# Kernel optimization log

Hardware: AMD Instinct MI355X
Metric: run time of the kernel (lower is better)

Reference implementation:

```python
import jax, jax.numpy as jnp
import numpy as np

V, H, L, B, S = 32000, 1024, 2, 8, 256


def setup_inputs() -> dict:
    key = jax.random.key(0)
    ks = jax.random.split(key, 12)
    s = 1.0 / np.sqrt(H)  # PyTorch LSTM/Linear init range
    u = lambda k, shape: jax.random.uniform(k, shape, jnp.float32, -s, s)
    return {
        "x": jax.random.randint(ks[0], (B, S), 0, V, dtype=jnp.int32),
        "h0": jnp.zeros((L, B, H), jnp.float32),
        "c0": jnp.zeros((L, B, H), jnp.float32),
        "w_ih0": u(ks[1], (4 * H, V)),
        "w_hh0": u(ks[2], (4 * H, H)),
        "b_ih0": u(ks[3], (4 * H,)),
        "b_hh0": u(ks[4], (4 * H,)),
        "w_ih1": u(ks[5], (4 * H, H)),
        "w_hh1": u(ks[6], (4 * H, H)),
        "b_ih1": u(ks[7], (4 * H,)),
        "b_hh1": u(ks[8], (4 * H,)),
        "fc_w": u(ks[9], (V, H)),
        "fc_b": u(ks[10], (V,)),
    }


def _lstm_layer(xproj, h0, c0, w_hh):
    """xproj: [S,B,4H] input-to-gate projection (biases folded in).
    Gate order i,f,g,o matches PyTorch."""
    def step(carry, xp):
        h, c = carry
        g = xp + h @ w_hh.T  # [B,4H]
        i, f, gg, o = jnp.split(g, 4, axis=-1)
        c = jax.nn.sigmoid(f) * c + jax.nn.sigmoid(i) * jnp.tanh(gg)
        h = jax.nn.sigmoid(o) * jnp.tanh(c)
        return (h, c), h
    (hT, cT), hs = jax.lax.scan(step, (h0, c0), xproj)
    return hs, hT, cT


def reference(x, h0, c0, w_ih0, w_hh0, b_ih0, b_hh0, w_ih1, w_hh1, b_ih1, b_hh1, fc_w, fc_b):
    # F.one_hot(x, V).float() @ w_ih0.T  ==  gather of rows of w_ih0.T (identical math)
    xp0 = jnp.take(w_ih0.T, x, axis=0) + (b_ih0 + b_hh0)  # [B,S,4H]
    xp0 = xp0.transpose(1, 0, 2)  # [S,B,4H] for time-major scan
    h1s, h1T, c1T = _lstm_layer(xp0, h0[0], c0[0], w_hh0)
    xp1 = h1s @ w_ih1.T + (b_ih1 + b_hh1)  # [S,B,4H]
    h2s, h2T, c2T = _lstm_layer(xp1, h0[1], c0[1], w_hh1)
    out = h2s.transpose(1, 0, 2).reshape(-1, H)  # [B*S,H]
    logits = out @ fc_w.T + fc_b  # [B*S,V]
    hn = jnp.stack([h1T, h2T])
    cn = jnp.stack([c1T, c2T])
    return logits, (hn, cn)
```

## Files before the change

kernel.cpp:

```cpp
#include <hip/hip_runtime.h>
#include <cmath>

typedef float  f32x4  __attribute__((ext_vector_type(4)));
typedef float  f32x2  __attribute__((ext_vector_type(2)));
typedef __bf16 bf16x8 __attribute__((ext_vector_type(8)));

static constexpr int HN  = 1024;
static constexpr int VN  = 32000;
static constexpr int BN  = 8;
static constexpr int SN  = 256;
static constexpr int H4N = 4096;

__global__ __launch_bounds__(256) void k_gather(const int* __restrict__ x,
    const float* __restrict__ w_ih0, const float* __restrict__ b_ih0,
    const float* __restrict__ b_hh0, float* __restrict__ xpB) {
  int t = blockIdx.x;
  __shared__ int toks[8];
  if (threadIdx.x < 8) toks[threadIdx.x] = x[threadIdx.x * SN + t];
  __syncthreads();
  int wgx = threadIdx.x;
  for (int g = 0; g < 4; ++g) {
    float vals[4][8];
    #pragma unroll
    for (int u = 0; u < 4; ++u) {
      int row = g * 1024 + wgx * 4 + u;
      float bias = b_ih0[row] + b_hh0[row];
      const float* wr = w_ih0 + (size_t)row * VN;
      #pragma unroll
      for (int b = 0; b < 8; ++b) vals[u][b] = wr[toks[b]] + bias;
    }
    float* dst = xpB + (((size_t)t * 256 + wgx) * 16 + g * 4) * 8;
    #pragma unroll
    for (int u = 0; u < 4; ++u) {
      *(f32x4*)&dst[u * 8]     = *(f32x4*)&vals[u][0];
      *(f32x4*)&dst[u * 8 + 4] = *(f32x4*)&vals[u][4];
    }
  }
}

__global__ __launch_bounds__(256, 1) void k_lstm(
    const float* __restrict__ xpB,
    const float* __restrict__ w_hh,
    const float* __restrict__ h0,
    const float* __restrict__ c0,
    float* __restrict__ hs,
    float* __restrict__ hn, float* __restrict__ cn,
    unsigned* __restrict__ bar) {
  __shared__ float wL[16][1024];
  __shared__ float hL[8192];
  __shared__ float gates[16][8];

  const int tid = threadIdx.x;
  const int wg  = blockIdx.x;
  const int u0  = wg * 4;

  for (int it = 0; it < 16; ++it) {
    int g = it >> 2, u = it & 3;
    int k4 = tid;
    int k4s = k4 ^ ((k4 >> 3) & 7);
    f32x4 v = *(const f32x4*)&w_hh[((size_t)g * HN + u0 + u) * HN + k4 * 4];
    *(f32x4*)&wL[it][k4s * 4] = v;
  }
  float c_reg = 0.f;
  if (tid < 32) c_reg = c0[(tid & 7) * HN + u0 + (tid >> 3)];

  const int ks = tid & 31, rg = (tid >> 5) & 3, bg = tid >> 7;
  const int ksx = ks & 7;
  const int hb = tid & 7;
  const int hk = tid >> 3;
  const int ku = ks >> 2, kb = ks & 3;
  const int lrow = rg * 4 + ku, lb = bg * 4 + kb;
  __syncthreads();

  for (int t = 0; t < SN; ++t) {
    float xpv = 0.f;
    if (ks < 16) xpv = xpB[((size_t)t * 256 + wg) * 128 + lrow * 8 + lb];

    if (t > 0) {
      if (tid < 64) {
        unsigned tgt = 4u * (unsigned)t;
        while (__hip_atomic_load(&bar[tid * 32], __ATOMIC_RELAXED,
                                 __HIP_MEMORY_SCOPE_AGENT) < tgt)
          __builtin_amdgcn_s_sleep(1);
      }
      __syncthreads();
    }

    unsigned long long rv[16];
    if (t == 0) {
      const unsigned long long* s8 =
          (const unsigned long long*)h0 + (size_t)hb * 512 + hk;
      #pragma unroll
      for (int j = 0; j < 16; ++j) rv[j] = s8[j * 32];
    } else {
      const unsigned long long* hsrc8 =
          (const unsigned long long*)(hs + (size_t)(t - 1) * (BN * HN))
          + (size_t)hb * 512 + hk;
      #pragma unroll
      for (int j = 0; j < 16; ++j)
        rv[j] = __hip_atomic_load((unsigned long long*)(hsrc8 + j * 32),
                                  __ATOMIC_RELAXED, __HIP_MEMORY_SCOPE_AGENT);
    }
    #pragma unroll
    for (int j = 0; j < 16; ++j) {
      int k64 = hk + j * 32;
      int k4 = k64 >> 1, half = k64 & 1;
      int idx = ((k4 << 3) | hb) ^ ((k4 >> 3) & 7);
      *(f32x2*)&hL[idx * 4 + half * 2] = __builtin_bit_cast(f32x2, rv[j]);
    }
    __syncthreads();

    float acc[4][4] = {};
    #pragma unroll
    for (int j = 0; j < 8; ++j) {
      int k4 = ks * 8 + j;
      int k4s = k4 ^ ksx;
      f32x4 wv[4], hv[4];
      #pragma unroll
      for (int ri = 0; ri < 4; ++ri)
        wv[ri] = *(const f32x4*)&wL[rg * 4 + ri][k4s * 4];
      #pragma unroll
      for (int bi = 0; bi < 4; ++bi) {
        int idx = ((k4 << 3) | (bg * 4 + bi)) ^ ksx;
        hv[bi] = *(const f32x4*)&hL[idx * 4];
      }
      #pragma unroll
      for (int ri = 0; ri < 4; ++ri)
        #pragma unroll
        for (int bi = 0; bi < 4; ++bi)
          acc[ri][bi] += wv[ri][0]*hv[bi][0] + wv[ri][1]*hv[bi][1]
                       + wv[ri][2]*hv[bi][2] + wv[ri][3]*hv[bi][3];
    }

    #pragma unroll
    for (int m = 1; m <= 16; m <<= 1)
      #pragma unroll
      for (int ri = 0; ri < 4; ++ri)
        #pragma unroll
        for (int bi = 0; bi < 4; ++bi)
          acc[ri][bi] += __shfl_xor(acc[ri][bi], m);

    if (ks < 16) gates[lrow][lb] = acc[ku][kb] + xpv;
    __syncthreads();

    if (tid < 32) {
      int u = tid >> 3, b = tid & 7;
      float gi = gates[0 * 4 + u][b], gf = gates[1 * 4 + u][b];
      float gg = gates[2 * 4 + u][b], go = gates[3 * 4 + u][b];
      float si = 1.f / (1.f + expf(-gi));
      float sf = 1.f / (1.f + expf(-gf));
      float so = 1.f / (1.f + expf(-go));
      c_reg = sf * c_reg + si * tanhf(gg);
      float h = so * tanhf(c_reg);
      __hip_atomic_store(&hs[(size_t)t * (BN * HN) + b * HN + u0 + u], h,
                         __ATOMIC_RELAXED, __HIP_MEMORY_SCOPE_AGENT);
      if (t == SN - 1) {
        hn[b * HN + u0 + u] = h;
        cn[b * HN + u0 + u] = c_reg;
      }
    }

    if (t != SN - 1) {
      if (tid == 0) {
        asm volatile("s_waitcnt vmcnt(0)" ::: "memory");
        __hip_atomic_fetch_add(&bar[(wg >> 2) * 32], 1u,
                               __ATOMIC_RELAXED, __HIP_MEMORY_SCOPE_AGENT);
      }
      __syncthreads();
    } else {
      __syncthreads();
    }
  }
}

__global__ __launch_bounds__(256) void k_split(const float* __restrict__ src,
    __bf16* __restrict__ hi, __bf16* __restrict__ lo) {
  int i = (blockIdx.x * 256 + threadIdx.x) * 4;
  f32x4 v = *(const f32x4*)&src[i];
  #pragma unroll
  for (int j = 0; j < 4; ++j) {
    __bf16 h = (__bf16)v[j];
    hi[i + j] = h;
    lo[i + j] = (__bf16)(v[j] - (float)h);
  }
}

__global__ __launch_bounds__(256) void k_gemm(const __bf16* __restrict__ Ahi,
    const __bf16* __restrict__ Alo, const float* __restrict__ Bsrc,
    const float* __restrict__ bias1, const float* __restrict__ bias2,
    float* __restrict__ C, int Mt, int N, int mode) {
  __shared__ __bf16 sAh[128][32], sAl[128][32], sBh[128][32], sBl[128][32];
  int bid = blockIdx.x;
  int tn = bid / Mt, tm = bid % Mt;
  int tid = threadIdx.x, lane = tid & 63, wid = tid >> 6;
  int wr = wid >> 1, wc = wid & 1;
  f32x4 acc[4][4] = {};
  const size_t K = 1024;

  for (int kk = 0; kk < 1024; kk += 32) {
    __syncthreads();
    #pragma unroll
    for (int it = 0; it < 2; ++it) {
      int c = it * 256 + tid;
      int r = c >> 2, k8 = (c & 3) * 8;
      size_t ga = (size_t)(tm * 128 + r) * K + kk + k8;
      *(bf16x8*)&sAh[r][k8] = *(const bf16x8*)&Ahi[ga];
      *(bf16x8*)&sAl[r][k8] = *(const bf16x8*)&Alo[ga];
      size_t gb = (size_t)(tn * 128 + r) * K + kk + k8;
      f32x4 x0 = *(const f32x4*)&Bsrc[gb];
      f32x4 x1 = *(const f32x4*)&Bsrc[gb + 4];
      bf16x8 bh, bl;
      #pragma unroll
      for (int j = 0; j < 4; ++j) {
        __bf16 h0 = (__bf16)x0[j]; bh[j]     = h0; bl[j]     = (__bf16)(x0[j] - (float)h0);
        __bf16 h1 = (__bf16)x1[j]; bh[4 + j] = h1; bl[4 + j] = (__bf16)(x1[j] - (float)h1);
      }
      *(bf16x8*)&sBh[r][k8] = bh;
      *(bf16x8*)&sBl[r][k8] = bl;
    }
    __syncthreads();

    int kq = (lane >> 4) * 8;
    bf16x8 ah[4], al[4], bh[4], bl[4];
    #pragma unroll
    for (int i = 0; i < 4; ++i) {
      int ra = wr * 64 + i * 16 + (lane & 15);
      ah[i] = *(const bf16x8*)&sAh[ra][kq];
      al[i] = *(const bf16x8*)&sAl[ra][kq];
      int rb = wc * 64 + i * 16 + (lane & 15);
      bh[i] = *(const bf16x8*)&sBh[rb][kq];
      bl[i] = *(const bf16x8*)&sBl[rb][kq];
    }
    #pragma unroll
    for (int i = 0; i < 4; ++i)
      #pragma unroll
      for (int j = 0; j < 4; ++j) {
        acc[i][j] = __builtin_amdgcn_mfma_f32_16x16x32_bf16(ah[i], bh[j], acc[i][j], 0, 0, 0);
        acc[i][j] = __builtin_amdgcn_mfma_f32_16x16x32_bf16(ah[i], bl[j], acc[i][j], 0, 0, 0);
        acc[i][j] = __builtin_amdgcn_mfma_f32_16x16x32_bf16(al[i], bh[j], acc[i][j], 0, 0, 0);
      }
  }

  #pragma unroll
  for (int j = 0; j < 4; ++j) {
    int gcol = tn * 128 + wc * 64 + j * 16 + (lane & 15);
    float bv = bias1[gcol] + (bias2 ? bias2[gcol] : 0.f);
    #pragma unroll
    for (int i = 0; i < 4; ++i) {
      #pragma unroll
      for (int r = 0; r < 4; ++r) {
        int row = tm * 128 + wr * 64 + i * 16 + ((lane >> 4) << 2) + r;
        float val = acc[i][j][r] + bv;
        if (mode == 2) {
          int t = row >> 3, b = row & 7;
          int g = gcol >> 10, rem = gcol & 1023, wgx = rem >> 2, u = rem & 3;
          C[(((size_t)t * 256 + wgx) * 16 + g * 4 + u) * 8 + b] = val;
        } else {
          int orow = (mode == 1) ? ((row & 7) * 256 + (row >> 3)) : row;
          C[(size_t)orow * N + gcol] = val;
        }
      }
    }
  }
}

extern "C" void kernel_launch(void* const* d_in, const int* in_sizes, int n_in,
                              void* d_out, int out_size, void* d_ws, size_t ws_size,
                              hipStream_t stream) {
  (void)in_sizes; (void)n_in; (void)out_size; (void)ws_size;
  const int*   x     = (const int*)  d_in[0];
  const float* h0    = (const float*)d_in[1];
  const float* c0    = (const float*)d_in[2];
  const float* w_ih0 = (const float*)d_in[3];
  const float* w_hh0 = (const float*)d_in[4];
  const float* b_ih0 = (const float*)d_in[5];
  const float* b_hh0 = (const float*)d_in[6];
  const float* w_ih1 = (const float*)d_in[7];
  const float* w_hh1 = (const float*)d_in[8];
  const float* b_ih1 = (const float*)d_in[9];
  const float* b_hh1 = (const float*)d_in[10];
  const float* fc_w  = (const float*)d_in[11];
  const float* fc_b  = (const float*)d_in[12];
  float* out = (float*)d_out;
  float* ws  = (float*)d_ws;

  float* xpB  = ws;
  float* h1s  = ws + 8388608;
  float* h2s  = ws + 10485760;
  __bf16* Ahi = (__bf16*)(ws + 12582912);
  __bf16* Alo = (__bf16*)(ws + 13631488);
  unsigned* bar = (unsigned*)(ws + 14680064);

  const size_t LOG = (size_t)2048 * VN;
  float* hn = out + LOG;
  float* cn = out + LOG + 16384;

  hipMemsetAsync(bar, 0, 4096 * sizeof(unsigned), stream);

  k_gather<<<SN, 256, 0, stream>>>(x, w_ih0, b_ih0, b_hh0, xpB);

  k_lstm<<<256, 256, 0, stream>>>(xpB, w_hh0, h0, c0, h1s, hn, cn, bar);

  k_split<<<2048, 256, 0, stream>>>(h1s, Ahi, Alo);
  k_gemm<<<16 * 32, 256, 0, stream>>>(Ahi, Alo, w_ih1, b_ih1, b_hh1, xpB,
                                      16, H4N, 2);

  k_lstm<<<256, 256, 0, stream>>>(xpB, w_hh1, h0 + BN * HN, c0 + BN * HN,
                                  h2s, hn + BN * HN, cn + BN * HN, bar + 2048);

  k_split<<<2048, 256, 0, stream>>>(h2s, Ahi, Alo);
  k_gemm<<<16 * 250, 256, 0, stream>>>(Ahi, Alo, fc_w, fc_b, nullptr, out,
                                       16, VN, 1);
}
```

Measured before the change: 5.261 ms.

## Split LSTM recurrence into two batch halves with separate grid barriers

The persistent LSTM kernel now processes each timestep as two half-batch chunks (4 batch rows each), each with its own global barrier counter set. Blocks that finish one half can signal and begin the other while stragglers are still on the first, overlapping barrier latency with compute. The cross-lane shuffle reduction is replaced by a shared-memory reduction buffer. The cost is twice as many barrier rounds and __syncthreads per step, plus a serial 32-term sum per gate element.

```diff
diff --git a/kernel.cpp b/kernel.cpp
--- a/kernel.cpp
+++ b/kernel.cpp
@@ -47,8 +47,9 @@
     float* __restrict__ hn, float* __restrict__ cn,
     unsigned* __restrict__ bar) {
   __shared__ float wL[16][1024];
-  __shared__ float hL[8192];
-  __shared__ float gates[16][8];
+  __shared__ float hL[4096];
+  __shared__ float red[8][4][2][32];
+  __shared__ float gates[16][4];
 
   const int tid = threadIdx.x;
   const int wg  = blockIdx.x;
@@ -61,113 +62,126 @@
     f32x4 v = *(const f32x4*)&w_hh[((size_t)g * HN + u0 + u) * HN + k4 * 4];
     *(f32x4*)&wL[it][k4s * 4] = v;
   }
-  float c_reg = 0.f;
-  if (tid < 32) c_reg = c0[(tid & 7) * HN + u0 + (tid >> 3)];
+  float cstA = 0.f, cstB = 0.f;
+  if (tid < 16) {
+    int u = tid >> 2, b4 = tid & 3;
+    cstA = c0[b4 * HN + u0 + u];
+    cstB = c0[(b4 + 4) * HN + u0 + u];
+  }
 
   const int ks = tid & 31, rg = (tid >> 5) & 3, bg = tid >> 7;
   const int ksx = ks & 7;
-  const int hb = tid & 7;
-  const int hk = tid >> 3;
-  const int ku = ks >> 2, kb = ks & 3;
-  const int lrow = rg * 4 + ku, lb = bg * 4 + kb;
+  const int lb4 = tid & 3, hk8 = tid >> 2;
+  const int prow = tid >> 2, pb4 = tid & 3;
   __syncthreads();
 
   for (int t = 0; t < SN; ++t) {
-    float xpv = 0.f;
-    if (ks < 16) xpv = xpB[((size_t)t * 256 + wg) * 128 + lrow * 8 + lb];
-
-    if (t > 0) {
+    #pragma unroll
+    for (int c = 0; c < 2; ++c) {
+      float xpv = 0.f;
+      if (tid < 64)
+        xpv = xpB[(((size_t)t * 256 + wg) * 16 + prow) * 8 + pb4 + c * 4];
+
+      if (t > 0) {
+        if (tid < 64) {
+          const unsigned* ctr = &bar[c * 2048 + tid * 32];
+          unsigned tgt = 4u * (unsigned)t;
+          while (__hip_atomic_load(ctr, __ATOMIC_RELAXED,
+                                   __HIP_MEMORY_SCOPE_AGENT) < tgt)
+            __builtin_amdgcn_s_sleep(1);
+        }
+        __syncthreads();
+      }
+
+      unsigned long long rv[8];
+      {
+        int hb = lb4 + c * 4;
+        if (t == 0) {
+          const unsigned long long* s8 =
+              (const unsigned long long*)h0 + (size_t)hb * 512 + hk8;
+          #pragma unroll
+          for (int j = 0; j < 8; ++j) rv[j] = s8[j * 64];
+        } else {
+          const unsigned long long* s8 =
+              (const unsigned long long*)(hs + (size_t)(t - 1) * (BN * HN))
+              + (size_t)hb * 512 + hk8;
+          #pragma unroll
+          for (int j = 0; j < 8; ++j)
+            rv[j] = __hip_atomic_load((unsigned long long*)(s8 + j * 64),
+                                      __ATOMIC_RELAXED,
+                                      __HIP_MEMORY_SCOPE_AGENT);
+        }
+      }
+      #pragma unroll
+      for (int j = 0; j < 8; ++j) {
+        int k64 = hk8 + j * 64;
+        int k4 = k64 >> 1, half = k64 & 1;
+        int idx = ((k4 << 2) | lb4) ^ ((k4 >> 3) & 7);
+        *(f32x2*)&hL[idx * 4 + half * 2] = __builtin_bit_cast(f32x2, rv[j]);
+      }
+      __syncthreads();
+
+      float acc[4][2] = {};
+      #pragma unroll
+      for (int j = 0; j < 8; ++j) {
+        int k4 = ks * 8 + j;
+        int k4s = k4 ^ ksx;
+        f32x4 wv[4], hv[2];
+        #pragma unroll
+        for (int ri = 0; ri < 4; ++ri)
+          wv[ri] = *(const f32x4*)&wL[rg * 4 + ri][k4s * 4];
+        #pragma unroll
+        for (int bi = 0; bi < 2; ++bi) {
+          int idx = ((k4 << 2) | (bg * 2 + bi)) ^ ksx;
+          hv[bi] = *(const f32x4*)&hL[idx * 4];
+        }
+        #pragma unroll
+        for (int ri = 0; ri < 4; ++ri)
+          #pragma unroll
+          for (int bi = 0; bi < 2; ++bi)
+            acc[ri][bi] += wv[ri][0]*hv[bi][0] + wv[ri][1]*hv[bi][1]
+                         + wv[ri][2]*hv[bi][2] + wv[ri][3]*hv[bi][3];
+      }
+      #pragma unroll
+      for (int ri = 0; ri < 4; ++ri)
+        #pragma unroll
+        for (int bi = 0; bi < 2; ++bi)
+          red[rg * 2 + bg][ri][bi][ks] = acc[ri][bi];
+      __syncthreads();
+
       if (tid < 64) {
-        unsigned tgt = 4u * (unsigned)t;
-        while (__hip_atomic_load(&bar[tid * 32], __ATOMIC_RELAXED,
-                                 __HIP_MEMORY_SCOPE_AGENT) < tgt)
-          __builtin_amdgcn_s_sleep(1);
+        int rrg = prow >> 2, ri = prow & 3, bbg = pb4 >> 1, bi = pb4 & 1;
+        const float* rp = red[rrg * 2 + bbg][ri][bi];
+        float s = 0.f;
+        #pragma unroll
+        for (int q = 0; q < 32; ++q) s += rp[(q + tid) & 31];
+        gates[prow][pb4] = s + xpv;
       }
       __syncthreads();
-    }
-
-    unsigned long long rv[16];
-    if (t == 0) {
-      const unsigned long long* s8 =
-          (const unsigned long long*)h0 + (size_t)hb * 512 + hk;
-      #pragma unroll
-      for (int j = 0; j < 16; ++j) rv[j] = s8[j * 32];
-    } else {
-      const unsigned long long* hsrc8 =
-          (const unsigned long long*)(hs + (size_t)(t - 1) * (BN * HN))
-          + (size_t)hb * 512 + hk;
-      #pragma unroll
-      for (int j = 0; j < 16; ++j)
-        rv[j] = __hip_atomic_load((unsigned long long*)(hsrc8 + j * 32),
-                                  __ATOMIC_RELAXED, __HIP_MEMORY_SCOPE_AGENT);
-    }
-    #pragma unroll
-    for (int j = 0; j < 16; ++j) {
-      int k64 = hk + j * 32;
-      int k4 = k64 >> 1, half = k64 & 1;
-      int idx = ((k4 << 3) | hb) ^ ((k4 >> 3) & 7);
-      *(f32x2*)&hL[idx * 4 + half * 2] = __builtin_bit_cast(f32x2, rv[j]);
-    }
-    __syncthreads();
-
-    float acc[4][4] = {};
-    #pragma unroll
-    for (int j = 0; j < 8; ++j) {
-      int k4 = ks * 8 + j;
-      int k4s = k4 ^ ksx;
-      f32x4 wv[4], hv[4];
-      #pragma unroll
-      for (int ri = 0; ri < 4; ++ri)
-        wv[ri] = *(const f32x4*)&wL[rg * 4 + ri][k4s * 4];
-      #pragma unroll
-      for (int bi = 0; bi < 4; ++bi) {
-        int idx = ((k4 << 3) | (bg * 4 + bi)) ^ ksx;
-        hv[bi] = *(const f32x4*)&hL[idx * 4];
-      }
-      #pragma unroll
-      for (int ri = 0; ri < 4; ++ri)
-        #pragma unroll
-        for (int bi = 0; bi < 4; ++bi)
-          acc[ri][bi] += wv[ri][0]*hv[bi][0] + wv[ri][1]*hv[bi][1]
-                       + wv[ri][2]*hv[bi][2] + wv[ri][3]*hv[bi][3];
-    }
-
-    #pragma unroll
-    for (int m = 1; m <= 16; m <<= 1)
-      #pragma unroll
-      for (int ri = 0; ri < 4; ++ri)
-        #pragma unroll
-        for (int bi = 0; bi < 4; ++bi)
-          acc[ri][bi] += __shfl_xor(acc[ri][bi], m);
-
-    if (ks < 16) gates[lrow][lb] = acc[ku][kb] + xpv;
-    __syncthreads();
-
-    if (tid < 32) {
-      int u = tid >> 3, b = tid & 7;
-      float gi = gates[0 * 4 + u][b], gf = gates[1 * 4 + u][b];
-      float gg = gates[2 * 4 + u][b], go = gates[3 * 4 + u][b];
-      float si = 1.f / (1.f + expf(-gi));
-      float sf = 1.f / (1.f + expf(-gf));
-      float so = 1.f / (1.f + expf(-go));
-      c_reg = sf * c_reg + si * tanhf(gg);
-      float h = so * tanhf(c_reg);
-      __hip_atomic_store(&hs[(size_t)t * (BN * HN) + b * HN + u0 + u], h,
-                         __ATOMIC_RELAXED, __HIP_MEMORY_SCOPE_AGENT);
-      if (t == SN - 1) {
-        hn[b * HN + u0 + u] = h;
-        cn[b * HN + u0 + u] = c_reg;
-      }
-    }
-
-    if (t != SN - 1) {
-      if (tid == 0) {
+
+      if (tid < 16) {
+        int u = tid >> 2, b4 = tid & 3, b = b4 + c * 4;
+        float gi = gates[0 * 4 + u][b4], gf = gates[1 * 4 + u][b4];
+        float gg = gates[2 * 4 + u][b4], go = gates[3 * 4 + u][b4];
+        float si = 1.f / (1.f + expf(-gi));
+        float sf = 1.f / (1.f + expf(-gf));
+        float so = 1.f / (1.f + expf(-go));
+        float cc = (c == 0) ? cstA : cstB;
+        cc = sf * cc + si * tanhf(gg);
+        float h = so * tanhf(cc);
+        if (c == 0) cstA = cc; else cstB = cc;
+        __hip_atomic_store(&hs[(size_t)t * (BN * HN) + b * HN + u0 + u], h,
+                           __ATOMIC_RELAXED, __HIP_MEMORY_SCOPE_AGENT);
+        if (t == SN - 1) {
+          hn[b * HN + u0 + u] = h;
+          cn[b * HN + u0 + u] = cc;
+        }
+      }
+      if (t != SN - 1 && tid == 0) {
         asm volatile("s_waitcnt vmcnt(0)" ::: "memory");
-        __hip_atomic_fetch_add(&bar[(wg >> 2) * 32], 1u,
+        __hip_atomic_fetch_add(&bar[c * 2048 + (wg >> 2) * 32], 1u,
                                __ATOMIC_RELAXED, __HIP_MEMORY_SCOPE_AGENT);
       }
-      __syncthreads();
-    } else {
       __syncthreads();
     }
   }
@@ -295,7 +309,7 @@
   float* hn = out + LOG;
   float* cn = out + LOG + 16384;
 
-  hipMemsetAsync(bar, 0, 4096 * sizeof(unsigned), stream);
+  hipMemsetAsync(bar, 0, 8192 * sizeof(unsigned), stream);
 
   k_gather<<<SN, 256, 0, stream>>>(x, w_ih0, b_ih0, b_hh0, xpB);
 
@@ -306,7 +320,7 @@
                                       16, H4N, 2);
 
   k_lstm<<<256, 256, 0, stream>>>(xpB, w_hh1, h0 + BN * HN, c0 + BN * HN,
-                                  h2s, hn + BN * HN, cn + BN * HN, bar + 2048);
+                                  h2s, hn + BN * HN, cn + BN * HN, bar + 4096);
 
   k_split<<<2048, 256, 0, stream>>>(h2s, Ahi, Alo);
   k_gemm<<<16 * 250, 256, 0, stream>>>(Ahi, Alo, fc_w, fc_b, nullptr, out,
```

Result: faster. 4.289 ms (-18.5%).

## Replace counter barrier with sentinel-flagged hidden state polling and LDS reduction

Applied to the files above, without the earlier changes.

The per-step cross-workgroup barrier (atomic counters plus spin-wait) is removed. The hidden-state buffers are prefilled with 0xFF (NaN sentinel) and each workgroup instead spins directly on the previous step's h values until none equal the sentinel. The shuffle-xor cross-lane reduction is also replaced with a shared-memory reduction buffer summed by 128 threads. This cuts one global round-trip per step, at the cost of two extra memsets, repeated 16-load polling, and an additional __syncthreads.

```diff
diff --git a/kernel.cpp b/kernel.cpp
--- a/kernel.cpp
+++ b/kernel.cpp
@@ -44,10 +44,10 @@
     const float* __restrict__ h0,
     const float* __restrict__ c0,
     float* __restrict__ hs,
-    float* __restrict__ hn, float* __restrict__ cn,
-    unsigned* __restrict__ bar) {
+    float* __restrict__ hn, float* __restrict__ cn) {
   __shared__ float wL[16][1024];
   __shared__ float hL[8192];
+  __shared__ float red[8][4][4][32];
   __shared__ float gates[16][8];
 
   const int tid = threadIdx.x;
@@ -68,23 +68,13 @@
   const int ksx = ks & 7;
   const int hb = tid & 7;
   const int hk = tid >> 3;
-  const int ku = ks >> 2, kb = ks & 3;
-  const int lrow = rg * 4 + ku, lb = bg * 4 + kb;
+  const int prow = tid >> 3, pb = tid & 7;
   __syncthreads();
 
   for (int t = 0; t < SN; ++t) {
     float xpv = 0.f;
-    if (ks < 16) xpv = xpB[((size_t)t * 256 + wg) * 128 + lrow * 8 + lb];
-
-    if (t > 0) {
-      if (tid < 64) {
-        unsigned tgt = 4u * (unsigned)t;
-        while (__hip_atomic_load(&bar[tid * 32], __ATOMIC_RELAXED,
-                                 __HIP_MEMORY_SCOPE_AGENT) < tgt)
-          __builtin_amdgcn_s_sleep(1);
-      }
-      __syncthreads();
-    }
+    if (tid < 128)
+      xpv = xpB[(((size_t)t * 256 + wg) * 16 + prow) * 8 + pb];
 
     unsigned long long rv[16];
     if (t == 0) {
@@ -93,13 +83,23 @@
       #pragma unroll
       for (int j = 0; j < 16; ++j) rv[j] = s8[j * 32];
     } else {
-      const unsigned long long* hsrc8 =
+      const unsigned long long* s8 =
           (const unsigned long long*)(hs + (size_t)(t - 1) * (BN * HN))
           + (size_t)hb * 512 + hk;
-      #pragma unroll
-      for (int j = 0; j < 16; ++j)
-        rv[j] = __hip_atomic_load((unsigned long long*)(hsrc8 + j * 32),
-                                  __ATOMIC_RELAXED, __HIP_MEMORY_SCOPE_AGENT);
+      while (true) {
+        #pragma unroll
+        for (int j = 0; j < 16; ++j)
+          rv[j] = __hip_atomic_load((unsigned long long*)(s8 + j * 32),
+                                    __ATOMIC_RELAXED, __HIP_MEMORY_SCOPE_AGENT);
+        unsigned bad = 0u;
+        #pragma unroll
+        for (int j = 0; j < 16; ++j) {
+          bad |= (unsigned)((unsigned)rv[j] == 0xFFFFFFFFu);
+          bad |= (unsigned)((unsigned)(rv[j] >> 32) == 0xFFFFFFFFu);
+        }
+        if (!bad) break;
+        __builtin_amdgcn_s_sleep(1);
+      }
     }
     #pragma unroll
     for (int j = 0; j < 16; ++j) {
@@ -131,16 +131,21 @@
           acc[ri][bi] += wv[ri][0]*hv[bi][0] + wv[ri][1]*hv[bi][1]
                        + wv[ri][2]*hv[bi][2] + wv[ri][3]*hv[bi][3];
     }
-
-    #pragma unroll
-    for (int m = 1; m <= 16; m <<= 1)
-      #pragma unroll
-      for (int ri = 0; ri < 4; ++ri)
-        #pragma unroll
-        for (int bi = 0; bi < 4; ++bi)
-          acc[ri][bi] += __shfl_xor(acc[ri][bi], m);
-
-    if (ks < 16) gates[lrow][lb] = acc[ku][kb] + xpv;
+    #pragma unroll
+    for (int ri = 0; ri < 4; ++ri)
+      #pragma unroll
+      for (int bi = 0; bi < 4; ++bi)
+        red[rg * 2 + bg][ri][bi][ks] = acc[ri][bi];
+    __syncthreads();
+
+    if (tid < 128) {
+      int rrg = prow >> 2, ri = prow & 3, bbg = pb >> 2, bi = pb & 3;
+      const float* rp = red[rrg * 2 + bbg][ri][bi];
+      float s = 0.f;
+      #pragma unroll
+      for (int q = 0; q < 32; ++q) s += rp[(q + tid) & 31];
+      gates[prow][pb] = s + xpv;
+    }
     __syncthreads();
 
     if (tid < 32) {
@@ -159,17 +164,7 @@
         cn[b * HN + u0 + u] = c_reg;
       }
     }
-
-    if (t != SN - 1) {
-      if (tid == 0) {
-        asm volatile("s_waitcnt vmcnt(0)" ::: "memory");
-        __hip_atomic_fetch_add(&bar[(wg >> 2) * 32], 1u,
-                               __ATOMIC_RELAXED, __HIP_MEMORY_SCOPE_AGENT);
-      }
-      __syncthreads();
-    } else {
-      __syncthreads();
-    }
+    __syncthreads();
   }
 }
 
@@ -289,24 +284,24 @@
   float* h2s  = ws + 10485760;
   __bf16* Ahi = (__bf16*)(ws + 12582912);
   __bf16* Alo = (__bf16*)(ws + 13631488);
-  unsigned* bar = (unsigned*)(ws + 14680064);
 
   const size_t LOG = (size_t)2048 * VN;
   float* hn = out + LOG;
   float* cn = out + LOG + 16384;
 
-  hipMemsetAsync(bar, 0, 4096 * sizeof(unsigned), stream);
+  hipMemsetAsync(h1s, 0xFF, (size_t)SN * BN * HN * 4, stream);
+  hipMemsetAsync(h2s, 0xFF, (size_t)SN * BN * HN * 4, stream);
 
   k_gather<<<SN, 256, 0, stream>>>(x, w_ih0, b_ih0, b_hh0, xpB);
 
-  k_lstm<<<256, 256, 0, stream>>>(xpB, w_hh0, h0, c0, h1s, hn, cn, bar);
+  k_lstm<<<256, 256, 0, stream>>>(xpB, w_hh0, h0, c0, h1s, hn, cn);
 
   k_split<<<2048, 256, 0, stream>>>(h1s, Ahi, Alo);
   k_gemm<<<16 * 32, 256, 0, stream>>>(Ahi, Alo, w_ih1, b_ih1, b_hh1, xpB,
                                       16, H4N, 2);
 
   k_lstm<<<256, 256, 0, stream>>>(xpB, w_hh1, h0 + BN * HN, c0 + BN * HN,
-                                  h2s, hn + BN * HN, cn + BN * HN, bar + 2048);
+                                  h2s, hn + BN * HN, cn + BN * HN);
 
   k_split<<<2048, 256, 0, stream>>>(h2s, Ahi, Alo);
   k_gemm<<<16 * 250, 256, 0, stream>>>(Ahi, Alo, fc_w, fc_b, nullptr, out,
```

New measurement: 4.425 ms. 15.9% less time.
